# Optimization experiments

Measured on AMD Instinct MI355X. Metric: run time of the kernel, lower is better.

Reference implementation:

```python
import math
import jax, jax.numpy as jnp
import numpy as np

D_MODEL = 1024
N_HEADS = 16
D_HEAD = D_MODEL // N_HEADS
BLOCK = 2048
BATCH = 2
SEQ = 2048


def setup_inputs() -> dict:
    key = jax.random.key(0)
    k1, k2, k3 = jax.random.split(key, 3)
    x = jax.random.normal(k1, (BATCH, SEQ, D_MODEL), dtype=jnp.float32)
    Wqkv = jax.random.normal(k2, (3 * D_MODEL, D_MODEL), dtype=jnp.float32) * 0.02
    Wo = jax.random.normal(k3, (D_MODEL, D_MODEL), dtype=jnp.float32) * 0.02
    # xi_init defaults to block/2
    log_xi = jnp.full((N_HEADS,), math.log(BLOCK / 2.0), dtype=jnp.float32)
    pi_gate_logit = jnp.full((N_HEADS,), 2.0, dtype=jnp.float32)
    e_gate_logit = jnp.full((N_HEADS,), 2.0, dtype=jnp.float32)
    return {"x": x, "Wqkv": Wqkv, "Wo": Wo, "log_xi": log_xi,
            "pi_gate_logit": pi_gate_logit, "e_gate_logit": e_gate_logit}


def _rotate(t, cos, sin):
    # t: (b, H, n, dh); cos/sin: (H, n, dh//2)
    t1 = t[..., 0::2]
    t2 = t[..., 1::2]
    r1 = t1 * cos - t2 * sin
    r2 = t1 * sin + t2 * cos
    # re-interleave even/odd lanes
    return jnp.stack([r1, r2], axis=-1).reshape(t.shape)


def reference(x, Wqkv, Wo, log_xi, pi_gate_logit, e_gate_logit):
    b, n, d = x.shape
    H, dh = N_HEADS, D_HEAD
    qkv = (x @ Wqkv.T).reshape(b, n, 3, H, dh)
    q = jnp.transpose(qkv[:, :, 0], (0, 2, 1, 3))  # (b,H,n,dh)
    k = jnp.transpose(qkv[:, :, 1], (0, 2, 1, 3))
    v = jnp.transpose(qkv[:, :, 2], (0, 2, 1, 3))

    pi_g = jax.nn.sigmoid(pi_gate_logit)  # (H,)
    e_g = jax.nn.sigmoid(e_gate_logit)    # (H,)

    kfrac = jnp.arange(0, dh, 2, dtype=jnp.float32) / dh
    pi_inv_freq = jnp.float32(math.pi) ** (1.0 - kfrac)  # (dh//2,)
    pos = jnp.arange(n, dtype=jnp.float32)
    theta = pos[:, None] * pi_inv_freq[None, :]           # (n, dh//2)
    theta = theta[None, :, :] * pi_g[:, None, None]       # (H, n, dh//2)
    cos, sin = jnp.cos(theta), jnp.sin(theta)

    q_rot = _rotate(q, cos, sin)
    k_rot = _rotate(k, cos, sin)

    scores = jnp.einsum('bhqd,bhkd->bhqk', q_rot, k_rot) / jnp.float32(math.sqrt(dh))

    xi = jnp.exp(log_xi)  # (H,)
    i = jnp.arange(n, dtype=jnp.float32)
    d_mat = jnp.abs(i[:, None] - i[None, :])              # (n, n)
    decay_bias = -(d_mat[None, :, :] / xi[:, None, None]) * e_g[:, None, None]  # (H,n,n)
    scores = scores + decay_bias[None]

    causal = jnp.tril(jnp.ones((n, n), dtype=bool))
    scores = jnp.where(causal[None, None], scores, jnp.float32(-jnp.inf))
    attn = jax.nn.softmax(scores, axis=-1)

    out = jnp.einsum('bhqk,bhkd->bhqd', attn, v)
    out = jnp.transpose(out, (0, 2, 1, 3)).reshape(b, n, d)
    return out @ Wo.T
```

## Files before the change

kernel.cpp:

```cpp
#include <hip/hip_runtime.h>

typedef unsigned short u16;
typedef unsigned int u32;
typedef __bf16 bf16x8 __attribute__((ext_vector_type(8)));
typedef float f32x4 __attribute__((ext_vector_type(4)));
typedef u16 u16x4 __attribute__((ext_vector_type(4)));

#define S_LEN 2048
#define NH 16
#define DH 64
#define DM 1024

#define GLDS(gp, lp) __builtin_amdgcn_global_load_lds( \
    (const __attribute__((address_space(1))) void*)(gp), \
    (__attribute__((address_space(3))) void*)(lp), 16, 0, 0)

__device__ __forceinline__ u16 f2bf(float f) {
  unsigned u = __float_as_uint(f);
  u += 0x7FFFu + ((u >> 16) & 1u);
  return (u16)(u >> 16);
}
__device__ __forceinline__ float bf2f(u16 h) {
  return __uint_as_float(((unsigned)h) << 16);
}

__global__ __launch_bounds__(256) void conv3_kernel(const float* __restrict__ a,
                                                    const float* __restrict__ wb,
                                                    const float* __restrict__ wc,
                                                    u16* __restrict__ oa,
                                                    u16* __restrict__ ob,
                                                    u16* __restrict__ oc) {
  int bid = blockIdx.x;
  const float* in;
  u16* out;
  int idx;
  if (bid < 2048)      { in = a;  out = oa; idx = bid; }
  else if (bid < 3584) { in = wb; out = ob; idx = bid - 2048; }
  else                 { in = wc; out = oc; idx = bid - 3584; }
  int i = idx * 2048 + threadIdx.x * 8;
  float4 v0 = *(const float4*)(in + i);
  float4 v1 = *(const float4*)(in + i + 4);
  u16x4 o0, o1;
  o0.x = f2bf(v0.x); o0.y = f2bf(v0.y); o0.z = f2bf(v0.z); o0.w = f2bf(v0.w);
  o1.x = f2bf(v1.x); o1.y = f2bf(v1.y); o1.z = f2bf(v1.z); o1.w = f2bf(v1.w);
  *(u16x4*)(out + i) = o0;
  *(u16x4*)(out + i + 4) = o1;
}

template <int MODE>
__global__ __launch_bounds__(256) void gemm_bt(const u16* __restrict__ A,
                                               const u16* __restrict__ B,
                                               void* __restrict__ C,
                                               int N, int K,
                                               const float* __restrict__ pi_gate_logit,
                                               u16* __restrict__ qrot,
                                               u16* __restrict__ krot,
                                               u16* __restrict__ vtp) {
  __shared__ __align__(16) u16 smem[24576];
  int tid = threadIdx.x;
  int w = tid >> 6, l = tid & 63, lg = l >> 4, lr = l & 15;

  int nwg = gridDim.x * gridDim.y;
  int lid = blockIdx.y * gridDim.x + blockIdx.x;
  int swz = (lid & 7) * (nwg >> 3) + (lid >> 3);
  int bx = swz % gridDim.x, by = swz / gridDim.x;
  int m0 = by * 128, n0 = bx * 128;

  int wm = (w >> 1) * 64, wn = (w & 1) * 64;
  int NK = K >> 5;

  int srow0 = w * 16 + (l >> 2);
  int srow1 = srow0 + 64;
  int scol = (l & 3) * 8;
  const u16* gA0 = A + (size_t)(m0 + srow0) * K + scol;
  const u16* gA1 = A + (size_t)(m0 + srow1) * K + scol;
  const u16* gB0 = B + (size_t)(n0 + srow0) * K + scol;
  const u16* gB1 = B + (size_t)(n0 + srow1) * K + scol;

  auto stage = [&](int bufi) {
    u16* ab = smem + bufi * 8192;
    u16* bb = ab + 4096;
    GLDS(gA0, ab + w * 512);
    GLDS(gA1, ab + (4 + w) * 512);
    GLDS(gB0, bb + w * 512);
    GLDS(gB1, bb + (4 + w) * 512);
    gA0 += 32; gA1 += 32; gB0 += 32; gB1 += 32;
  };

  f32x4 zero4 = {0.f, 0.f, 0.f, 0.f};
  f32x4 acc[4][4];
#pragma unroll
  for (int mt = 0; mt < 4; ++mt)
#pragma unroll
    for (int nt = 0; nt < 4; ++nt) acc[mt][nt] = zero4;

  stage(0);
  stage(1);

  int p = 0;
  int pn = 2;
  for (int kt = 0; kt < NK; ++kt) {
    if (kt + 1 < NK) asm volatile("s_waitcnt vmcnt(4)" ::: "memory");
    else             asm volatile("s_waitcnt vmcnt(0)" ::: "memory");
    __builtin_amdgcn_s_barrier();
    __builtin_amdgcn_sched_barrier(0);
    if (kt + 2 < NK) {
      stage(pn);
      pn = (pn == 2) ? 0 : pn + 1;
    }

    const u16* ab = smem + p * 8192;
    const u16* bb = ab + 4096;
    bf16x8 af[4], bfr[4];
#pragma unroll
    for (int mt = 0; mt < 4; ++mt)
      af[mt] = *(const bf16x8*)(ab + (wm + mt * 16 + lr) * 32 + lg * 8);
#pragma unroll
    for (int nt = 0; nt < 4; ++nt)
      bfr[nt] = *(const bf16x8*)(bb + (wn + nt * 16 + lr) * 32 + lg * 8);
    __builtin_amdgcn_s_setprio(1);
#pragma unroll
    for (int mt = 0; mt < 4; ++mt)
#pragma unroll
      for (int nt = 0; nt < 4; ++nt)
        acc[mt][nt] = __builtin_amdgcn_mfma_f32_16x16x32_bf16(af[mt], bfr[nt], acc[mt][nt], 0, 0, 0);
    __builtin_amdgcn_s_setprio(0);

    p = (p == 2) ? 0 : p + 1;
  }

  if constexpr (MODE != 2) {
#pragma unroll
    for (int mt = 0; mt < 4; ++mt)
#pragma unroll
      for (int nt = 0; nt < 4; ++nt)
#pragma unroll
        for (int r = 0; r < 4; ++r) {
          int row = m0 + wm + mt * 16 + lg * 4 + r;
          int col = n0 + wn + nt * 16 + lr;
          float v = acc[mt][nt][r];
          if (MODE == 1) ((float*)C)[(size_t)row * N + col] = v;
          else           ((u16*)C)[(size_t)row * N + col] = f2bf(v);
        }
  } else {
    int region = n0 >> 10;
    int hh = ((n0 + wn) >> 6) & 15;
    if (region < 2) {
      float pg = 1.0f / (1.0f + __expf(-pi_gate_logit[hh]));
      float sc = region ? 1.0f : 0.18033688011111772f;
      u16* dst = region ? krot : qrot;
      float cfreq[4];
#pragma unroll
      for (int nt = 0; nt < 4; ++nt) {
        float pp = (float)((nt * 16 + lr) >> 1);
        cfreq[nt] = exp2f((1.0f - pp * 0.03125f) * 1.6514961294723187f) * pg;
      }
#pragma unroll
      for (int mt = 0; mt < 4; ++mt)
#pragma unroll
        for (int r = 0; r < 4; ++r) {
          int row = m0 + wm + mt * 16 + lg * 4 + r;
          int s = row & 2047, bb2 = row >> 11;
          size_t base = ((size_t)((bb2 * 16 + hh) * 2048 + s)) * 64;
          float fs = (float)s;
#pragma unroll
          for (int nt = 0; nt < 4; ++nt) {
            float mine = acc[mt][nt][r];
            float other = __shfl_xor(mine, 1);
            float rev = fs * cfreq[nt] * 0.15915494309189535f;
            rev -= floorf(rev);
            float cs = __builtin_amdgcn_cosf(rev);
            float sn = __builtin_amdgcn_sinf(rev);
            float rot = (lr & 1) ? (other * sn + mine * cs)
                                 : (mine * cs - other * sn);
            dst[base + nt * 16 + lr] = f2bf(rot * sc);
          }
        }
    } else {
#pragma unroll
      for (int mt = 0; mt < 4; ++mt)
#pragma unroll
        for (int nt = 0; nt < 4; ++nt) {
          int row0r = m0 + wm + mt * 16 + lg * 4;
          int s = row0r & 2047, bb2 = row0r >> 11;
          int d = nt * 16 + lr;
          u16x4 o;
          o.x = f2bf(acc[mt][nt][0]); o.y = f2bf(acc[mt][nt][1]);
          o.z = f2bf(acc[mt][nt][2]); o.w = f2bf(acc[mt][nt][3]);
          *(u16x4*)(vtp + ((size_t)((bb2 * 16 + hh) * 64 + d)) * 2048 + s) = o;
        }
    }
  }
}

template <bool DIAG>
__device__ __forceinline__ void attn_tile(const unsigned char* __restrict__ kbuf,
                                          const unsigned char* __restrict__ vbuf,
                                          float mt, const float (&cbv)[16],
                                          const bf16x8 (&qf)[2],
                                          f32x4 (&oacc)[4],
                                          float& mrun, float& lrun,
                                          int lg, int lr, int il,
                                          unsigned char* pbuf) {
  f32x4 sacc[4];
#pragma unroll
  for (int nt = 0; nt < 4; ++nt)
#pragma unroll
    for (int r = 0; r < 4; ++r) sacc[nt][r] = cbv[nt * 4 + r] + mt;
  __builtin_amdgcn_s_setprio(1);
#pragma unroll
  for (int nt = 0; nt < 4; ++nt)
#pragma unroll
    for (int kk = 0; kk < 2; ++kk) {
      int row = nt * 16 + lr;
      int sl_ = lg + kk * 4;
      bf16x8 kf = *(const bf16x8*)(kbuf + row * 128 + ((sl_ ^ (row & 7)) << 4));
      sacc[nt] = __builtin_amdgcn_mfma_f32_16x16x32_bf16(kf, qf[kk], sacc[nt], 0, 0, 0);
    }
  __builtin_amdgcn_s_setprio(0);

  float pv[16];
#pragma unroll
  for (int nt = 0; nt < 4; ++nt)
#pragma unroll
    for (int r = 0; r < 4; ++r) {
      float v = sacc[nt][r];
      if (DIAG) {
        int jl = nt * 16 + lg * 4 + r;
        v = (jl <= il) ? v : -1e30f;
      }
      pv[nt * 4 + r] = v;
    }

  float m1 = pv[0];
#pragma unroll
  for (int i = 1; i < 16; ++i) m1 = fmaxf(m1, pv[i]);
  m1 = fmaxf(m1, __shfl_xor(m1, 16));
  m1 = fmaxf(m1, __shfl_xor(m1, 32));

  if (__ballot(m1 > 8.f)) {
    float d = fmaxf(m1, 0.f);
    float fac = __builtin_amdgcn_exp2f(-d);
    mrun += d;
    lrun *= fac;
    int fi = __float_as_int(fac);
    float facr[4];
#pragma unroll
    for (int r = 0; r < 4; ++r)
      facr[r] = __int_as_float(__builtin_amdgcn_ds_bpermute((4 * lg + r) << 2, fi));
#pragma unroll
    for (int nt = 0; nt < 4; ++nt)
#pragma unroll
      for (int r = 0; r < 4; ++r) oacc[nt][r] *= facr[r];
#pragma unroll
    for (int i = 0; i < 16; ++i) pv[i] -= d;
  }

  float p[16];
  float rsum = 0.f;
#pragma unroll
  for (int i = 0; i < 16; ++i) {
    p[i] = __builtin_amdgcn_exp2f(pv[i]);
    rsum += p[i];
  }
  rsum += __shfl_xor(rsum, 16);
  rsum += __shfl_xor(rsum, 32);
  lrun += rsum;

#pragma unroll
  for (int nt = 0; nt < 4; ++nt)
#pragma unroll
    for (int rp = 0; rp < 2; ++rp) {
      u32 pk;
      asm("v_cvt_pk_bf16_f32 %0, %1, %2" : "=v"(pk)
          : "v"(p[nt * 4 + 2 * rp]), "v"(p[nt * 4 + 2 * rp + 1]));
      *(u32*)(pbuf + ((lr * 128 + nt * 32 + lg * 8 + rp * 4) ^ ((lr & 7) << 4))) = pk;
    }
  asm volatile("s_waitcnt lgkmcnt(0)" ::: "memory");

  bf16x8 pf[2];
#pragma unroll
  for (int kk = 0; kk < 2; ++kk)
    pf[kk] = *(const bf16x8*)(pbuf + ((lr * 128 + (lg + 4 * kk) * 16) ^ ((lr & 7) << 4)));

  __builtin_amdgcn_s_setprio(1);
#pragma unroll
  for (int nt = 0; nt < 4; ++nt)
#pragma unroll
    for (int kk = 0; kk < 2; ++kk) {
      int row = nt * 16 + lr;
      int sl_ = lg + kk * 4;
      bf16x8 vf = *(const bf16x8*)(vbuf + row * 128 + ((sl_ ^ (row & 7)) << 4));
      oacc[nt] = __builtin_amdgcn_mfma_f32_16x16x32_bf16(pf[kk], vf, oacc[nt], 0, 0, 0);
    }
  __builtin_amdgcn_s_setprio(0);
}

__global__ __launch_bounds__(256, 3) void attn_kernel(const u16* __restrict__ qrot,
                                                      const u16* __restrict__ krot,
                                                      const u16* __restrict__ vt,
                                                      const float* __restrict__ log_xi,
                                                      const float* __restrict__ e_gate_logit,
                                                      u16* __restrict__ attnout) {
  int bh = blockIdx.x;
  int qt = 31 - blockIdx.y;
  int b = bh >> 4, h = bh & 15;
  int tid = threadIdx.x, w = tid >> 6, l = tid & 63, lg = l >> 4, lr = l & 15;
  int q0 = qt * 64;
  int il = w * 16 + lr;

  const float L2E = 1.4426950408889634f;
  float eg = 1.0f / (1.0f + __expf(-e_gate_logit[h]));
  float cdec2 = eg * __expf(-log_xi[h]) * L2E;

  __shared__ __align__(16) unsigned char smem[40960];
  unsigned char* pbuf = smem + 32768 + (w << 11);

  const size_t bhS = (size_t)bh * S_LEN;
  const u16* kb0 = krot + bhS * DH;
  const u16* vb0 = vt + (size_t)bh * DH * S_LEN;

  bf16x8 qf[2];
  {
    const u16* qp = qrot + (bhS + q0 + il) * DH + lg * 8;
    qf[0] = *(const bf16x8*)(qp);
    qf[1] = *(const bf16x8*)(qp + 32);
  }

  float cbv[16];
#pragma unroll
  for (int nt = 0; nt < 4; ++nt)
#pragma unroll
    for (int r = 0; r < 4; ++r)
      cbv[nt * 4 + r] = (float)(nt * 16 + lg * 4 + r) * cdec2;

  int c0 = tid, c1 = 256 + tid;
  int row0 = c0 >> 3, sl0 = c0 & 7;
  int row1 = c1 >> 3, sl1 = c1 & 7;

  bf16x8 kr[2], vr[2];
  auto load_kv = [&](int t) {
    kr[0] = *(const bf16x8*)(kb0 + (size_t)(t * 64 + row0) * DH + sl0 * 8);
    kr[1] = *(const bf16x8*)(kb0 + (size_t)(t * 64 + row1) * DH + sl1 * 8);
    vr[0] = *(const bf16x8*)(vb0 + (size_t)row0 * S_LEN + t * 64 + sl0 * 8);
    vr[1] = *(const bf16x8*)(vb0 + (size_t)row1 * S_LEN + t * 64 + sl1 * 8);
  };
  auto stage = [&](int p) {
    unsigned char* kb = smem + p * 8192;
    unsigned char* vb = smem + 16384 + p * 8192;
    *(bf16x8*)(kb + row0 * 128 + ((sl0 ^ (row0 & 7)) << 4)) = kr[0];
    *(bf16x8*)(kb + row1 * 128 + ((sl1 ^ (row1 & 7)) << 4)) = kr[1];
    *(bf16x8*)(vb + row0 * 128 + ((sl0 ^ (row0 & 7)) << 4)) = vr[0];
    *(bf16x8*)(vb + row1 * 128 + ((sl1 ^ (row1 & 7)) << 4)) = vr[1];
  };

  f32x4 zero4 = {0.f, 0.f, 0.f, 0.f};
  f32x4 oacc[4];
#pragma unroll
  for (int nt = 0; nt < 4; ++nt) oacc[nt] = zero4;
  float mrun = 0.f, lrun = 0.f;

  load_kv(0);
  float step = 64.f * cdec2;
  float tb = 0.f;
  int p = 0;
  for (int t = 0; t < qt; ++t, tb += step, p ^= 1) {
    stage(p);
    load_kv(t + 1);
    __syncthreads();
    attn_tile<false>(smem + p * 8192, smem + 16384 + p * 8192, tb - mrun, cbv,
                     qf, oacc, mrun, lrun, lg, lr, il, pbuf);
  }
  stage(p);
  __syncthreads();
  attn_tile<true>(smem + p * 8192, smem + 16384 + p * 8192, tb - mrun, cbv,
                  qf, oacc, mrun, lrun, lg, lr, il, pbuf);

  float lfin[4];
  int li = __float_as_int(lrun);
#pragma unroll
  for (int r = 0; r < 4; ++r)
    lfin[r] = __int_as_float(__builtin_amdgcn_ds_bpermute((4 * lg + r) << 2, li));
#pragma unroll
  for (int nt = 0; nt < 4; ++nt)
#pragma unroll
    for (int r = 0; r < 4; ++r) {
      int srow = q0 + w * 16 + lg * 4 + r;
      int col = h * DH + nt * 16 + lr;
      attnout[((size_t)b * S_LEN + srow) * DM + col] = f2bf(oacc[nt][r] / lfin[r]);
    }
}

extern "C" void kernel_launch(void* const* d_in, const int* in_sizes, int n_in,
                              void* d_out, int out_size, void* d_ws, size_t ws_size,
                              hipStream_t stream) {
  const float* x    = (const float*)d_in[0];
  const float* Wqkv = (const float*)d_in[1];
  const float* Wo   = (const float*)d_in[2];
  const float* log_xi        = (const float*)d_in[3];
  const float* pi_gate_logit = (const float*)d_in[4];
  const float* e_gate_logit  = (const float*)d_in[5];

  u16* xb     = (u16*)d_ws;
  u16* wqkvb  = xb + 4194304;
  u16* wob    = wqkvb + 3145728;
  u16* qrot   = wob + 1048576;
  u16* krot   = qrot + 4194304;
  u16* vt     = krot + 4194304;
  u16* attno  = vt + 4194304;

  conv3_kernel<<<4096, 256, 0, stream>>>(x, Wqkv, Wo, xb, wqkvb, wob);

  gemm_bt<2><<<dim3(24, 32), 256, 0, stream>>>(xb, wqkvb, nullptr, 3072, 1024,
                                               pi_gate_logit, qrot, krot, vt);

  attn_kernel<<<dim3(32, 32), 256, 0, stream>>>(qrot, krot, vt, log_xi, e_gate_logit, attno);

  gemm_bt<1><<<dim3(8, 32), 256, 0, stream>>>(attno, wob, d_out, 1024, 1024,
                                              nullptr, nullptr, nullptr, nullptr);
}
```

Measured before the change: 102.1 us.

## Stage K/V tiles with async global_load_lds double buffering in attention kernel

Result: no change. 104.1 us (+1.9%).

```diff
diff --git a/kernel.cpp b/kernel.cpp
--- a/kernel.cpp
+++ b/kernel.cpp
@@ -296,7 +296,7 @@
   __builtin_amdgcn_s_setprio(0);
 }
 
-__global__ __launch_bounds__(256, 3) void attn_kernel(const u16* __restrict__ qrot,
+__global__ __launch_bounds__(256, 4) void attn_kernel(const u16* __restrict__ qrot,
                                                       const u16* __restrict__ krot,
                                                       const u16* __restrict__ vt,
                                                       const float* __restrict__ log_xi,
@@ -317,12 +317,10 @@
   unsigned char* pbuf = smem + 32768 + (w << 11);
 
   const size_t bhS = (size_t)bh * S_LEN;
-  const u16* kb0 = krot + bhS * DH;
-  const u16* vb0 = vt + (size_t)bh * DH * S_LEN;
 
   bf16x8 qf[2];
   {
-    const u16* qp = qrot + (bhS + q0 + il) * DH + lg * 8;
+    const u16* qp = qrot + (bhS + q0 + w * 16 + lr) * DH + lg * 8;
     qf[0] = *(const bf16x8*)(qp);
     qf[1] = *(const bf16x8*)(qp + 32);
   }
@@ -334,24 +332,22 @@
     for (int r = 0; r < 4; ++r)
       cbv[nt * 4 + r] = (float)(nt * 16 + lg * 4 + r) * cdec2;
 
-  int c0 = tid, c1 = 256 + tid;
-  int row0 = c0 >> 3, sl0 = c0 & 7;
-  int row1 = c1 >> 3, sl1 = c1 & 7;
-
-  bf16x8 kr[2], vr[2];
-  auto load_kv = [&](int t) {
-    kr[0] = *(const bf16x8*)(kb0 + (size_t)(t * 64 + row0) * DH + sl0 * 8);
-    kr[1] = *(const bf16x8*)(kb0 + (size_t)(t * 64 + row1) * DH + sl1 * 8);
-    vr[0] = *(const bf16x8*)(vb0 + (size_t)row0 * S_LEN + t * 64 + sl0 * 8);
-    vr[1] = *(const bf16x8*)(vb0 + (size_t)row1 * S_LEN + t * 64 + sl1 * 8);
-  };
-  auto stage = [&](int p) {
-    unsigned char* kb = smem + p * 8192;
-    unsigned char* vb = smem + 16384 + p * 8192;
-    *(bf16x8*)(kb + row0 * 128 + ((sl0 ^ (row0 & 7)) << 4)) = kr[0];
-    *(bf16x8*)(kb + row1 * 128 + ((sl1 ^ (row1 & 7)) << 4)) = kr[1];
-    *(bf16x8*)(vb + row0 * 128 + ((sl0 ^ (row0 & 7)) << 4)) = vr[0];
-    *(bf16x8*)(vb + row1 * 128 + ((sl1 ^ (row1 & 7)) << 4)) = vr[1];
+  int lrow = l >> 3;
+  int lswz = ((l & 7) ^ lrow) * 16;
+  const unsigned char* ksrc0 = (const unsigned char*)(krot + bhS * DH)
+                               + (w * 8 + lrow) * 128 + lswz;
+  const unsigned char* ksrc1 = ksrc0 + 32 * 128;
+  const unsigned char* vsrc0 = (const unsigned char*)(vt + (size_t)bh * DH * S_LEN)
+                               + (size_t)(w * 8 + lrow) * 4096 + lswz;
+  const unsigned char* vsrc1 = vsrc0 + (size_t)32 * 4096;
+
+  auto glds_stage = [&](int p, int t) {
+    unsigned char* kb = smem + p * 8192 + w * 1024;
+    unsigned char* vb = smem + 16384 + p * 8192 + w * 1024;
+    GLDS(ksrc0 + (size_t)t * 8192, kb);
+    GLDS(ksrc1 + (size_t)t * 8192, kb + 4096);
+    GLDS(vsrc0 + t * 128, vb);
+    GLDS(vsrc1 + t * 128, vb + 4096);
   };
 
   f32x4 zero4 = {0.f, 0.f, 0.f, 0.f};
@@ -360,19 +356,20 @@
   for (int nt = 0; nt < 4; ++nt) oacc[nt] = zero4;
   float mrun = 0.f, lrun = 0.f;
 
-  load_kv(0);
+  glds_stage(0, 0);
+  asm volatile("s_waitcnt vmcnt(0)" ::: "memory");
+  __builtin_amdgcn_s_barrier();
+
   float step = 64.f * cdec2;
   float tb = 0.f;
   int p = 0;
   for (int t = 0; t < qt; ++t, tb += step, p ^= 1) {
-    stage(p);
-    load_kv(t + 1);
-    __syncthreads();
+    glds_stage(p ^ 1, t + 1);
     attn_tile<false>(smem + p * 8192, smem + 16384 + p * 8192, tb - mrun, cbv,
                      qf, oacc, mrun, lrun, lg, lr, il, pbuf);
-  }
-  stage(p);
-  __syncthreads();
+    asm volatile("s_waitcnt vmcnt(0)" ::: "memory");
+    __builtin_amdgcn_s_barrier();
+  }
   attn_tile<true>(smem + p * 8192, smem + 16384 + p * 8192, tb - mrun, cbv,
                   qf, oacc, mrun, lrun, lg, lr, il, pbuf);
 
```
